# Performance work log

Hardware: AMD Instinct MI355X
Metric: run time of the kernel (lower is better)

The kernel has to match this reference:

```python
import jax, jax.numpy as jnp
import numpy as np

CARRY_DIM = 384
READ_DIM = 128
D_MODEL = CARRY_DIM + READ_DIM  # 512
VOCAB = 128
NUM_FF = 7
B, T = 128, 1024


def _pm1(key, shape):
    # random +/-1 floats, matching random_pm1 in the torch source
    return jnp.where(jax.random.bernoulli(key, 0.5, shape), 1.0, -1.0).astype(jnp.float32)


def setup_inputs() -> dict:
    key = jax.random.key(0)
    k0, k1, k2, k3, k4 = jax.random.split(key, 5)
    return {
        "tokens": jax.random.randint(k0, (B, T), 0, VOCAB, dtype=jnp.int32),
        "initial": _pm1(k1, (D_MODEL,)),
        "embed": _pm1(k2, (VOCAB, READ_DIM)),
        "ff": _pm1(k3, (NUM_FF, D_MODEL, D_MODEL)),
        "ff_thresh": jnp.zeros((NUM_FF, D_MODEL), jnp.float32),
        "head": _pm1(k4, (READ_DIM, VOCAB)),
    }


def reference(tokens, initial, embed, ff, ff_thresh, head):
    # tokens:[B,T] int32; all params are +/-1 floats (the unpacked view of the
    # bit-packed int32 buffers; popcount GEMM == +/-1 matmul in integer arithmetic).
    b = tokens.shape[0]
    emb = jnp.swapaxes(embed[tokens], 0, 1)          # [T,B,READ_DIM]
    state0 = jnp.broadcast_to(initial, (b, D_MODEL))  # [B,512] +/-1

    def step(state, e):
        # replace read slice with current token embedding
        x = jnp.concatenate([state[:, :CARRY_DIM], e], axis=1)  # [B,512]

        def layer(xc, wt):
            w, t = wt  # w:[512,512], t:[512]
            # binary matmul (popcount dot in +/-1 space) + threshold nonlinearity
            return jnp.where(xc @ w >= t, 1.0, -1.0).astype(jnp.float32), None

        x, _ = jax.lax.scan(layer, x, (ff, ff_thresh))
        logits = x[:, CARRY_DIM:] @ head  # [B,VOCAB] integer-valued counts
        return x, logits

    _, logits = jax.lax.scan(step, state0, emb)  # logits:[T,B,V]
    return jnp.swapaxes(logits, 0, 1)            # [B,T,V]
```

## Files before the change

### kernel.cpp

```cpp
#include <hip/hip_runtime.h>
#include <hip/hip_bf16.h>
#include <stdint.h>

#define NUM_FF 7
#define DM 512
#define CARRY 384
#define RD 128
#define VOCABN 128
#define BATCH 128
#define TLEN 1024

__global__ void pack_ff_kernel(const float* __restrict__ ff, uint32_t* __restrict__ ffp) {
    int idx = blockIdx.x * blockDim.x + threadIdx.x;
    if (idx >= NUM_FF * 16 * DM) return;
    int j = idx & (DM - 1);
    int k = (idx >> 9) & 15;
    int l = idx >> 13;
    const float* base = ff + (size_t)l * DM * DM + (size_t)(k * 32) * DM + j;
    uint32_t w = 0;
#pragma unroll
    for (int i = 0; i < 32; ++i)
        w |= (base[(size_t)i * DM] > 0.0f ? 1u : 0u) << i;
    ffp[idx] = w;
}

__global__ void pack_small_kernel(const float* __restrict__ embed,
                                  const float* __restrict__ head,
                                  const float* __restrict__ initial,
                                  uint32_t* __restrict__ embp,
                                  uint32_t* __restrict__ headp,
                                  uint32_t* __restrict__ initp) {
    int idx = threadIdx.x;
    {
        int v = idx >> 2, k = idx & 3;
        uint32_t w = 0;
#pragma unroll
        for (int i = 0; i < 32; ++i)
            w |= (embed[v * RD + k * 32 + i] > 0.0f ? 1u : 0u) << i;
        embp[idx] = w;
    }
    {
        int k = idx >> 7, v = idx & 127;
        uint32_t w = 0;
#pragma unroll
        for (int i = 0; i < 32; ++i)
            w |= (head[(k * 32 + i) * VOCABN + v] > 0.0f ? 1u : 0u) << i;
        headp[idx] = w;
    }
    if (idx < 16) {
        uint32_t w = 0;
#pragma unroll
        for (int i = 0; i < 32; ++i)
            w |= (initial[idx * 32 + i] > 0.0f ? 1u : 0u) << i;
        initp[idx] = w;
    }
}

__launch_bounds__(512, 2)
__global__ void brnn_kernel(const int* __restrict__ tokens,
                            const float* __restrict__ ff_thresh,
                            const uint32_t* __restrict__ ffp,
                            const uint32_t* __restrict__ embp,
                            const uint32_t* __restrict__ headp,
                            const uint32_t* __restrict__ initp,
                            float* __restrict__ out) {
    const int b = blockIdx.x;
    const int tid = threadIdx.x;
    const int wave = tid >> 6;
    const int lane = tid & 63;

    __shared__ uint32_t xbuf[2][16];
    __shared__ uint32_t hx[4];
    __shared__ uint32_t emb_lds[VOCABN * 4];
    __shared__ uint32_t head_lds[4 * VOCABN];
    __shared__ int tok_lds[TLEN];

    uint32_t w[NUM_FF][16];
#pragma unroll
    for (int l = 0; l < NUM_FF; ++l)
#pragma unroll
        for (int k = 0; k < 16; ++k)
            w[l][k] = ffp[l * (16 * DM) + k * DM + tid];
    float th[NUM_FF];
#pragma unroll
    for (int l = 0; l < NUM_FF; ++l)
        th[l] = ff_thresh[l * DM + tid];

    emb_lds[tid] = embp[tid];
    head_lds[tid] = headp[tid];
    tok_lds[tid] = tokens[b * TLEN + tid];
    tok_lds[tid + 512] = tokens[b * TLEN + tid + 512];
    if (tid < 16) xbuf[0][tid] = initp[tid];
    __syncthreads();
    if (tid < 4) xbuf[0][12 + tid] = emb_lds[tok_lds[0] * 4 + tid];
    __syncthreads();

    int p = 0;
    float* outb = out + (size_t)b * TLEN * VOCABN;

    for (int t = 0; t < TLEN; ++t) {
#pragma unroll
        for (int l = 0; l < NUM_FF; ++l) {
            const uint4* xb = (const uint4*)xbuf[p];
            uint4 xa = xb[0], xc = xb[1], xd = xb[2], xe = xb[3];
            int a0 = __popc(xa.x ^ w[l][0]);
            a0 += __popc(xa.y ^ w[l][1]);
            a0 += __popc(xa.z ^ w[l][2]);
            a0 += __popc(xa.w ^ w[l][3]);
            int a1 = __popc(xc.x ^ w[l][4]);
            a1 += __popc(xc.y ^ w[l][5]);
            a1 += __popc(xc.z ^ w[l][6]);
            a1 += __popc(xc.w ^ w[l][7]);
            int a2 = __popc(xd.x ^ w[l][8]);
            a2 += __popc(xd.y ^ w[l][9]);
            a2 += __popc(xd.z ^ w[l][10]);
            a2 += __popc(xd.w ^ w[l][11]);
            int a3 = __popc(xe.x ^ w[l][12]);
            a3 += __popc(xe.y ^ w[l][13]);
            a3 += __popc(xe.z ^ w[l][14]);
            a3 += __popc(xe.w ^ w[l][15]);
            int acc = (a0 + a1) + (a2 + a3);
            bool bit = (float)(DM - 2 * acc) >= th[l];
            unsigned long long m = __ballot(bit);
            if (l < NUM_FF - 1) {
                if (lane == 0) {
                    xbuf[p ^ 1][2 * wave] = (uint32_t)m;
                    xbuf[p ^ 1][2 * wave + 1] = (uint32_t)(m >> 32);
                }
            } else {
                if (lane == 0) {
                    if (wave < 6) {
                        xbuf[p ^ 1][2 * wave] = (uint32_t)m;
                        xbuf[p ^ 1][2 * wave + 1] = (uint32_t)(m >> 32);
                    } else {
                        hx[2 * (wave - 6)] = (uint32_t)m;
                        hx[2 * (wave - 6) + 1] = (uint32_t)(m >> 32);
                    }
                }
                if (tid < 4 && t + 1 < TLEN)
                    xbuf[p ^ 1][12 + tid] = emb_lds[tok_lds[t + 1] * 4 + tid];
            }
            __syncthreads();
            p ^= 1;
        }
        if (tid < VOCABN) {
            uint32_t h0 = head_lds[0 * VOCABN + tid];
            uint32_t h1 = head_lds[1 * VOCABN + tid];
            uint32_t h2 = head_lds[2 * VOCABN + tid];
            uint32_t h3 = head_lds[3 * VOCABN + tid];
            int hc = __popc(hx[0] ^ h0);
            hc += __popc(hx[1] ^ h1);
            hc += __popc(hx[2] ^ h2);
            hc += __popc(hx[3] ^ h3);
            outb[t * VOCABN + tid] = (float)(RD - 2 * hc);
        }
    }
}

extern "C" void kernel_launch(void* const* d_in, const int* in_sizes, int n_in,
                              void* d_out, int out_size, void* d_ws, size_t ws_size,
                              hipStream_t stream) {
    const int* tokens = (const int*)d_in[0];
    const float* initial = (const float*)d_in[1];
    const float* embed = (const float*)d_in[2];
    const float* ff = (const float*)d_in[3];
    const float* ff_thresh = (const float*)d_in[4];
    const float* head = (const float*)d_in[5];
    float* out = (float*)d_out;

    uint32_t* ffp = (uint32_t*)d_ws;
    uint32_t* embp = ffp + NUM_FF * 16 * DM;
    uint32_t* headp = embp + 512;
    uint32_t* initp = headp + 512;

    pack_ff_kernel<<<(NUM_FF * 16 * DM + 255) / 256, 256, 0, stream>>>(ff, ffp);
    pack_small_kernel<<<1, 512, 0, stream>>>(embed, head, initial, embp, headp, initp);
    brnn_kernel<<<BATCH, 512, 0, stream>>>(tokens, ff_thresh, ffp, embp, headp, initp, out);
}
```

Baseline: 1.939 ms.

## Halve block to 256 threads with two columns per thread and lighter barriers

Each thread now computes two output columns per layer, so the block shrinks from 8 waves to 4 and each per-layer barrier synchronises fewer waves. __syncthreads is replaced by an inline waitcnt plus s_barrier, and ballot results are stored as uint4 into ping-pong LDS buffers, with the time loop unrolled by two to remove buffer-index arithmetic. The head weights move from LDS into registers. This doubles per-thread register use (224 weight words) and work per thread, which risks spills or a longer critical path per layer.

```diff
diff --git a/kernel.cpp b/kernel.cpp
--- a/kernel.cpp
+++ b/kernel.cpp
@@ -56,7 +56,30 @@
     }
 }
 
-__launch_bounds__(512, 2)
+__device__ __forceinline__ int bdot16(uint4 s0, uint4 s1, uint4 s2, uint4 s3,
+                                      const uint32_t* __restrict__ w) {
+    int a = __popc(s0.x ^ w[0]);
+    a += __popc(s0.y ^ w[1]);
+    a += __popc(s0.z ^ w[2]);
+    a += __popc(s0.w ^ w[3]);
+    a += __popc(s1.x ^ w[4]);
+    a += __popc(s1.y ^ w[5]);
+    a += __popc(s1.z ^ w[6]);
+    a += __popc(s1.w ^ w[7]);
+    int b = __popc(s2.x ^ w[8]);
+    b += __popc(s2.y ^ w[9]);
+    b += __popc(s2.z ^ w[10]);
+    b += __popc(s2.w ^ w[11]);
+    b += __popc(s3.x ^ w[12]);
+    b += __popc(s3.y ^ w[13]);
+    b += __popc(s3.z ^ w[14]);
+    b += __popc(s3.w ^ w[15]);
+    return a + b;
+}
+
+#define SYNCB asm volatile("s_waitcnt lgkmcnt(0)\n\ts_barrier" ::: "memory")
+
+__launch_bounds__(256, 1)
 __global__ void brnn_kernel(const int* __restrict__ tokens,
                             const float* __restrict__ ff_thresh,
                             const uint32_t* __restrict__ ffp,
@@ -66,95 +89,110 @@
                             float* __restrict__ out) {
     const int b = blockIdx.x;
     const int tid = threadIdx.x;
-    const int wave = tid >> 6;
+    const int wv = tid >> 6;
     const int lane = tid & 63;
-
-    __shared__ uint32_t xbuf[2][16];
-    __shared__ uint32_t hx[4];
+    const int c0 = (wv << 7) | lane;
+    const int c1 = c0 + 64;
+
+    __shared__ uint4 xq0[4], xq1[4];
+    __shared__ uint4 hxv;
     __shared__ uint32_t emb_lds[VOCABN * 4];
-    __shared__ uint32_t head_lds[4 * VOCABN];
-    __shared__ int tok_lds[TLEN];
-
-    uint32_t w[NUM_FF][16];
+    __shared__ int tok_lds[TLEN + 4];
+
+    uint32_t wA[NUM_FF][16], wB[NUM_FF][16];
 #pragma unroll
     for (int l = 0; l < NUM_FF; ++l)
 #pragma unroll
-        for (int k = 0; k < 16; ++k)
-            w[l][k] = ffp[l * (16 * DM) + k * DM + tid];
-    float th[NUM_FF];
-#pragma unroll
-    for (int l = 0; l < NUM_FF; ++l)
-        th[l] = ff_thresh[l * DM + tid];
-
+        for (int k = 0; k < 16; ++k) {
+            wA[l][k] = ffp[l * (16 * DM) + k * DM + c0];
+            wB[l][k] = ffp[l * (16 * DM) + k * DM + c1];
+        }
+    float thA[NUM_FF], thB[NUM_FF];
+#pragma unroll
+    for (int l = 0; l < NUM_FF; ++l) {
+        thA[l] = ff_thresh[l * DM + c0];
+        thB[l] = ff_thresh[l * DM + c1];
+    }
+    uint32_t h0 = 0, h1 = 0, h2 = 0, h3 = 0;
+    if (tid < VOCABN) {
+        h0 = headp[0 * VOCABN + tid];
+        h1 = headp[1 * VOCABN + tid];
+        h2 = headp[2 * VOCABN + tid];
+        h3 = headp[3 * VOCABN + tid];
+    }
     emb_lds[tid] = embp[tid];
-    head_lds[tid] = headp[tid];
+    emb_lds[tid + 256] = embp[tid + 256];
     tok_lds[tid] = tokens[b * TLEN + tid];
+    tok_lds[tid + 256] = tokens[b * TLEN + tid + 256];
     tok_lds[tid + 512] = tokens[b * TLEN + tid + 512];
-    if (tid < 16) xbuf[0][tid] = initp[tid];
+    tok_lds[tid + 768] = tokens[b * TLEN + tid + 768];
+    if (tid == 0) tok_lds[TLEN] = 0;
+    if (tid < 16) ((uint32_t*)xq0)[tid] = initp[tid];
     __syncthreads();
-    if (tid < 4) xbuf[0][12 + tid] = emb_lds[tok_lds[0] * 4 + tid];
+    if (tid < 4) ((uint32_t*)xq0)[12 + tid] = emb_lds[tok_lds[0] * 4 + tid];
     __syncthreads();
 
-    int p = 0;
     float* outb = out + (size_t)b * TLEN * VOCABN;
 
-    for (int t = 0; t < TLEN; ++t) {
-#pragma unroll
-        for (int l = 0; l < NUM_FF; ++l) {
-            const uint4* xb = (const uint4*)xbuf[p];
-            uint4 xa = xb[0], xc = xb[1], xd = xb[2], xe = xb[3];
-            int a0 = __popc(xa.x ^ w[l][0]);
-            a0 += __popc(xa.y ^ w[l][1]);
-            a0 += __popc(xa.z ^ w[l][2]);
-            a0 += __popc(xa.w ^ w[l][3]);
-            int a1 = __popc(xc.x ^ w[l][4]);
-            a1 += __popc(xc.y ^ w[l][5]);
-            a1 += __popc(xc.z ^ w[l][6]);
-            a1 += __popc(xc.w ^ w[l][7]);
-            int a2 = __popc(xd.x ^ w[l][8]);
-            a2 += __popc(xd.y ^ w[l][9]);
-            a2 += __popc(xd.z ^ w[l][10]);
-            a2 += __popc(xd.w ^ w[l][11]);
-            int a3 = __popc(xe.x ^ w[l][12]);
-            a3 += __popc(xe.y ^ w[l][13]);
-            a3 += __popc(xe.z ^ w[l][14]);
-            a3 += __popc(xe.w ^ w[l][15]);
-            int acc = (a0 + a1) + (a2 + a3);
-            bool bit = (float)(DM - 2 * acc) >= th[l];
-            unsigned long long m = __ballot(bit);
-            if (l < NUM_FF - 1) {
-                if (lane == 0) {
-                    xbuf[p ^ 1][2 * wave] = (uint32_t)m;
-                    xbuf[p ^ 1][2 * wave + 1] = (uint32_t)(m >> 32);
-                }
-            } else {
-                if (lane == 0) {
-                    if (wave < 6) {
-                        xbuf[p ^ 1][2 * wave] = (uint32_t)m;
-                        xbuf[p ^ 1][2 * wave + 1] = (uint32_t)(m >> 32);
-                    } else {
-                        hx[2 * (wave - 6)] = (uint32_t)m;
-                        hx[2 * (wave - 6) + 1] = (uint32_t)(m >> 32);
-                    }
-                }
-                if (tid < 4 && t + 1 < TLEN)
-                    xbuf[p ^ 1][12 + tid] = emb_lds[tok_lds[t + 1] * 4 + tid];
-            }
-            __syncthreads();
-            p ^= 1;
-        }
-        if (tid < VOCABN) {
-            uint32_t h0 = head_lds[0 * VOCABN + tid];
-            uint32_t h1 = head_lds[1 * VOCABN + tid];
-            uint32_t h2 = head_lds[2 * VOCABN + tid];
-            uint32_t h3 = head_lds[3 * VOCABN + tid];
-            int hc = __popc(hx[0] ^ h0);
-            hc += __popc(hx[1] ^ h1);
-            hc += __popc(hx[2] ^ h2);
-            hc += __popc(hx[3] ^ h3);
-            outb[t * VOCABN + tid] = (float)(RD - 2 * hc);
-        }
-    }
+#define LAYER(l, SRCQ, DSTQ) do {                                              \
+        uint4 s0 = (SRCQ)[0], s1 = (SRCQ)[1], s2 = (SRCQ)[2], s3 = (SRCQ)[3]; \
+        int accA = bdot16(s0, s1, s2, s3, wA[l]);                              \
+        int accB = bdot16(s0, s1, s2, s3, wB[l]);                              \
+        unsigned long long m0 = __ballot((float)(DM - 2 * accA) >= thA[l]);    \
+        unsigned long long m1 = __ballot((float)(DM - 2 * accB) >= thB[l]);    \
+        if (lane == 0)                                                         \
+            (DSTQ)[wv] = make_uint4((uint32_t)m0, (uint32_t)(m0 >> 32),        \
+                                    (uint32_t)m1, (uint32_t)(m1 >> 32));       \
+        SYNCB;                                                                 \
+    } while (0)
+
+#define LAYERF(l, SRCQ, DSTQ, tnext) do {                                      \
+        uint4 s0 = (SRCQ)[0], s1 = (SRCQ)[1], s2 = (SRCQ)[2], s3 = (SRCQ)[3]; \
+        int accA = bdot16(s0, s1, s2, s3, wA[l]);                              \
+        int accB = bdot16(s0, s1, s2, s3, wB[l]);                              \
+        unsigned long long m0 = __ballot((float)(DM - 2 * accA) >= thA[l]);    \
+        unsigned long long m1 = __ballot((float)(DM - 2 * accB) >= thB[l]);    \
+        if (lane == 0) {                                                       \
+            uint4 v = make_uint4((uint32_t)m0, (uint32_t)(m0 >> 32),           \
+                                 (uint32_t)m1, (uint32_t)(m1 >> 32));          \
+            if (wv < 3) (DSTQ)[wv] = v;                                        \
+            else hxv = v;                                                      \
+        }                                                                      \
+        if (tid < 4)                                                           \
+            ((uint32_t*)(DSTQ))[12 + tid] = emb_lds[tok_lds[tnext] * 4 + tid]; \
+        SYNCB;                                                                 \
+    } while (0)
+
+#define HEADOUT(t) do {                                                        \
+        if (tid < VOCABN) {                                                    \
+            uint4 hv = hxv;                                                    \
+            int hc = __popc(hv.x ^ h0) + __popc(hv.y ^ h1) +                   \
+                     __popc(hv.z ^ h2) + __popc(hv.w ^ h3);                    \
+            outb[(t) * VOCABN + tid] = (float)(RD - 2 * hc);                   \
+        }                                                                      \
+    } while (0)
+
+    for (int t = 0; t < TLEN; t += 2) {
+        LAYER(0, xq0, xq1);
+        LAYER(1, xq1, xq0);
+        LAYER(2, xq0, xq1);
+        LAYER(3, xq1, xq0);
+        LAYER(4, xq0, xq1);
+        LAYER(5, xq1, xq0);
+        LAYERF(6, xq0, xq1, t + 1);
+        HEADOUT(t);
+        LAYER(0, xq1, xq0);
+        LAYER(1, xq0, xq1);
+        LAYER(2, xq1, xq0);
+        LAYER(3, xq0, xq1);
+        LAYER(4, xq1, xq0);
+        LAYER(5, xq0, xq1);
+        LAYERF(6, xq1, xq0, t + 2);
+        HEADOUT(t + 1);
+    }
+#undef LAYER
+#undef LAYERF
+#undef HEADOUT
 }
 
 extern "C" void kernel_launch(void* const* d_in, const int* in_sizes, int n_in,
@@ -175,5 +213,5 @@
 
     pack_ff_kernel<<<(NUM_FF * 16 * DM + 255) / 256, 256, 0, stream>>>(ff, ffp);
     pack_small_kernel<<<1, 512, 0, stream>>>(embed, head, initial, embp, headp, initp);
-    brnn_kernel<<<BATCH, 512, 0, stream>>>(tokens, ff_thresh, ffp, embp, headp, initp, out);
-}
+    brnn_kernel<<<BATCH, 256, 0, stream>>>(tokens, ff_thresh, ffp, embp, headp, initp, out);
+}
```

After: 2.198 ms. 13.3% more time.
